# Kernel optimization log

Measured on AMD Instinct MI355X. Metric: run time of the kernel, lower is better.

Reference implementation:

```python
import jax, jax.numpy as jnp
import numpy as np

EPS_LN = 1e-12
EPS_BN = 1e-5


def layernorm(x, w, b):
    u = jnp.mean(x, axis=-1, keepdims=True)
    s = jnp.mean((x - u) ** 2, axis=-1, keepdims=True)
    return w * ((x - u) / jnp.sqrt(s + EPS_LN)) + b


def reps_block(x, ln1_w, ln1_b, lin_w, lin_b, ln2_w, ln2_b):
    # GRAPHLayerNorm -> (dropout, identity in eval) -> Linear -> ReLU -> GRAPHLayerNorm
    h = layernorm(x, ln1_w, ln1_b)
    h = jax.nn.relu(jnp.einsum('bnd,od->bno', h, lin_w) + lin_b)
    return layernorm(h, ln2_w, ln2_b)


def attend(x):
    # full dense self-attention: softmax(x x^T) x ; dropout is identity in eval
    scores = jnp.einsum('bnd,bmd->bnm', x, x)  # [B,4096,4096]
    attn = jax.nn.softmax(scores, axis=-1)
    return jnp.einsum('bnm,bmd->bnd', attn, x)


def setup_inputs() -> dict:
    key = jax.random.key(0)
    ks = jax.random.split(key, 8)
    B, C, H, W = 4, 512, 64, 64
    D = 512
    inp = {
        'T1': jax.random.normal(ks[0], (B, C, H, W), jnp.float32),
        'T2': jax.random.normal(ks[1], (B, C, H, W), jnp.float32),
        'w_conv3': jax.random.normal(ks[2], (1024, 1024, 3, 3), jnp.float32) * 0.01,
        'w_conv1': jax.random.normal(ks[3], (512, 1024, 1, 1), jnp.float32) * 0.03,
        'bn_gamma': jnp.ones((512,), jnp.float32),
        'bn_beta': jnp.zeros((512,), jnp.float32),
        'bn_mean': jnp.zeros((512,), jnp.float32),
        'bn_var': jnp.ones((512,), jnp.float32),
        'ln1_w': jnp.ones((D,), jnp.float32),
        'ln1_b': jnp.zeros((D,), jnp.float32),
        'lin_w': jax.random.normal(ks[4], (D, D), jnp.float32) * 0.04,
        'lin_b': jnp.zeros((D,), jnp.float32),
        'ln2_w': jnp.ones((D,), jnp.float32),
        'ln2_b': jnp.zeros((D,), jnp.float32),
    }
    return inp


def reference(T1, T2, w_conv3, w_conv1, bn_gamma, bn_beta, bn_mean, bn_var,
              ln1_w, ln1_b, lin_w, lin_b, ln2_w, ln2_b):
    B = T1.shape[0]
    X = jnp.concatenate((T1, T2), axis=1)  # [B,1024,64,64]
    dn = ('NCHW', 'OIHW', 'NCHW')
    X = jax.lax.conv_general_dilated(X, w_conv3, (1, 1), ((1, 1), (1, 1)), dimension_numbers=dn)
    X = jax.lax.conv_general_dilated(X, w_conv1, (1, 1), ((0, 0), (0, 0)), dimension_numbers=dn)  # [B,512,64,64]
    # BatchNorm (eval, running stats) + ReLU
    inv = (bn_gamma / jnp.sqrt(bn_var + EPS_BN))[None, :, None, None]
    X = jax.nn.relu(X * inv + (bn_beta - bn_mean * bn_gamma / jnp.sqrt(bn_var + EPS_BN))[None, :, None, None])
    x = X.transpose(0, 2, 3, 1).reshape(B, 4096, 512)
    # block 1
    rel = attend(x)
    rel = reps_block(x + rel, ln1_w, ln1_b, lin_w, lin_b, ln2_w, ln2_b)
    # block 2 (original code reuses self.reps_graph, i.e. SAME params)
    rel1 = attend(rel)
    rel1 = reps_block(rel + rel1, ln1_w, ln1_b, lin_w, lin_b, ln2_w, ln2_b)
    return rel1.reshape(B, 64, 64, 512).transpose(0, 3, 1, 2)  # [B,512,64,64]
```

## Files before the change

### kernel.cpp

```cpp
#include <hip/hip_runtime.h>
#include <stdint.h>

typedef float f32x4 __attribute__((ext_vector_type(4)));
typedef __bf16 bf16x8 __attribute__((ext_vector_type(8)));
typedef unsigned short u16;
typedef unsigned short u16x8 __attribute__((ext_vector_type(8)));
typedef unsigned short u16x4 __attribute__((ext_vector_type(4)));

__device__ __forceinline__ float bf2f(u16 u){ unsigned int i = ((unsigned int)u)<<16; float f; __builtin_memcpy(&f,&i,4); return f; }
__device__ __forceinline__ u16 f2bf(float f){ unsigned int i; __builtin_memcpy(&i,&f,4); i += 0x7FFFu + ((i>>16)&1u); return (u16)(i>>16); }
__device__ __forceinline__ u16 f2h(float f){ _Float16 h = (_Float16)f; u16 b; __builtin_memcpy(&b,&h,2); return b; }
__device__ __forceinline__ float h2f(u16 b){ _Float16 h; __builtin_memcpy(&h,&b,2); return (float)h; }

__device__ __forceinline__ void gld16(const void* g, void* l){
  __builtin_amdgcn_global_load_lds(
      (const __attribute__((address_space(1))) void*)(uintptr_t)g,
      (__attribute__((address_space(3))) void*)(unsigned int)(uintptr_t)l, 16, 0, 0);
}

__global__ __launch_bounds__(256) void pad_interior(const float* __restrict__ T1,
                                                    const float* __restrict__ T2,
                                                    u16* __restrict__ Xpad){
  const int n = blockIdx.z, ct = blockIdx.y, pt = blockIdx.x;
  const int t = threadIdx.x;
  const int c0 = ct*64, p0 = pt*64;
  const float* src = (c0 < 512) ? (T1 + ((long)n*512 + c0)*4096)
                                : (T2 + ((long)n*512 + (c0-512))*4096);
  __shared__ u16 lds[64][66];
  #pragma unroll
  for (int i=0;i<4;i++){
    int c = i*16 + (t>>4);
    int ch = t&15;
    float4 v = *(const float4*)(src + (long)c*4096 + p0 + ch*4);
    int p = ch*4;
    lds[p+0][c] = f2bf(v.x); lds[p+1][c] = f2bf(v.y);
    lds[p+2][c] = f2bf(v.z); lds[p+3][c] = f2bf(v.w);
  }
  __syncthreads();
  #pragma unroll
  for (int i=0;i<8;i++){
    int p = i*8 + (t>>5);
    int c2 = t&31;
    int pix = p0 + p; int yy = (pix>>6)+1, xx = (pix&63)+1;
    ushort2 val; val.x = lds[p][2*c2]; val.y = lds[p][2*c2+1];
    *(ushort2*)(Xpad + (((long)n*66 + yy)*66 + xx)*1024 + c0 + 2*c2) = val;
  }
}

__global__ __launch_bounds__(256) void prep_w3(const float* __restrict__ w3, u16* __restrict__ wk3t){
  const int o = blockIdx.x; const int t = threadIdx.x;
  __shared__ u16 lds[9216];
  const float* src = w3 + (long)o*9216;
  #pragma unroll
  for (int i=0;i<9;i++){
    int j = i*256 + t;
    float4 v = *(const float4*)(src + j*4);
    lds[j*4+0]=f2bf(v.x); lds[j*4+1]=f2bf(v.y); lds[j*4+2]=f2bf(v.z); lds[j*4+3]=f2bf(v.w);
  }
  __syncthreads();
  u16* dst = wk3t + (long)o*9216;
  #pragma unroll
  for (int i=0;i<36;i++){
    int j = i*256 + t; int tp = j>>10, ci = j&1023;
    dst[j] = lds[ci*9+tp];
  }
}

__global__ void prep_w1(const float* __restrict__ w1, const float* __restrict__ bg,
                        const float* __restrict__ bv, u16* __restrict__ w1t){
  long i = (long)blockIdx.x*256 + threadIdx.x;
  int o = (int)(i>>10);
  float inv = bg[o] / sqrtf(bv[o] + 1e-5f);
  w1t[i] = f2bf(w1[i]*inv);
}

__global__ void prep_bias1(const float* __restrict__ bg, const float* __restrict__ bb,
                           const float* __restrict__ bm, const float* __restrict__ bv,
                           float* __restrict__ bias1){
  int o = blockIdx.x*256+threadIdx.x;
  float inv = bg[o]/sqrtf(bv[o]+1e-5f);
  bias1[o] = bb[o] - bm[o]*inv;
}

__global__ void cvt_bf(const float* __restrict__ s, u16* __restrict__ d){
  long i = (long)blockIdx.x*256 + threadIdx.x;
  d[i] = f2bf(s[i]);
}

__global__ __launch_bounds__(256) void row_norm(const u16* __restrict__ x, float* __restrict__ nrm){
  const int row = blockIdx.x*4 + (threadIdx.x>>6);
  const int lane = threadIdx.x & 63;
  u16x8 q = *(const u16x8*)(x + (long)row*512 + lane*8);
  float s = 0.f;
  #pragma unroll
  for (int j=0;j<8;j++){ float f = bf2f(q[j]); s += f*f; }
  #pragma unroll
  for (int off=32; off; off>>=1) s += __shfl_xor(s, off);
  if (lane==0) nrm[row] = s;
}

__global__ __launch_bounds__(256) void transpose_bf(const u16* __restrict__ src, u16* __restrict__ dst,
                                                    int R, int C, long sStr, long dStr){
  const int z = blockIdx.z;
  src += (long)z*sStr; dst += (long)z*dStr;
  const int r0 = blockIdx.x*64, c0 = blockIdx.y*64;
  const int t = threadIdx.x;
  __shared__ u16 lds[64][66];
  #pragma unroll
  for (int i=0;i<4;i++){
    int r = i*16 + (t>>4), ch = t&15;
    ushort4 v = *(const ushort4*)(src + (long)(r0+r)*C + c0 + ch*4);
    lds[r][ch*4+0]=v.x; lds[r][ch*4+1]=v.y; lds[r][ch*4+2]=v.z; lds[r][ch*4+3]=v.w;
  }
  __syncthreads();
  #pragma unroll
  for (int i=0;i<4;i++){
    int c = i*16 + (t>>4), ch = t&15;
    ushort4 v;
    v.x = lds[ch*4+0][c]; v.y = lds[ch*4+1][c]; v.z = lds[ch*4+2][c]; v.w = lds[ch*4+3][c];
    *(ushort4*)(dst + (long)(c0+c)*R + r0 + ch*4) = v;
  }
}

__global__ __launch_bounds__(256) void transpose_bf_f32(const u16* __restrict__ src, float* __restrict__ dst){
  const int z = blockIdx.z;
  src += (long)z*4096*512; dst += (long)z*512*4096;
  const int r0 = blockIdx.x*64, c0 = blockIdx.y*64;
  const int t = threadIdx.x;
  __shared__ u16 lds[64][66];
  #pragma unroll
  for (int i=0;i<4;i++){
    int r = i*16 + (t>>4), ch = t&15;
    ushort4 v = *(const ushort4*)(src + (long)(r0+r)*512 + c0 + ch*4);
    lds[r][ch*4+0]=v.x; lds[r][ch*4+1]=v.y; lds[r][ch*4+2]=v.z; lds[r][ch*4+3]=v.w;
  }
  __syncthreads();
  #pragma unroll
  for (int i=0;i<4;i++){
    int c = i*16 + (t>>4), ch = t&15;
    float4 v;
    v.x = bf2f(lds[ch*4+0][c]); v.y = bf2f(lds[ch*4+1][c]);
    v.z = bf2f(lds[ch*4+2][c]); v.w = bf2f(lds[ch*4+3][c]);
    *(float4*)(dst + (long)(c0+c)*4096 + r0 + ch*4) = v;
  }
}

template<int EPI, int CONV>
__global__ __launch_bounds__(512, 2) void gemm256(
    const u16* __restrict__ A, const u16* __restrict__ Bt, void* __restrict__ Cv,
    int K, int lda, int ldb, int ldc, const float* __restrict__ srow,
    float2* __restrict__ spart)
{
  extern __shared__ u16 sm[];
  const int t = threadIdx.x;
  const int lane = t & 63;
  const int wid = t >> 6;
  const int wr = wid >> 2, wc = wid & 3;

  const int orig = blockIdx.y * gridDim.x + blockIdx.x;
  const int cpx = (gridDim.x * gridDim.y) >> 3;
  const int swz = (orig & 7) * cpx + (orig >> 3);
  const int bx = swz % gridDim.x;
  const int by = swz / gridDim.x;
  const long m0 = (long)by * 256, n0 = (long)bx * 256;

  const int row0 = t >> 2;
  const int cs0  = (t & 3) ^ ((row0 >> 1) & 3);

  const u16 *aB0, *aB1;
  if (CONV) {
    long m_ = m0 + row0;
    long pb0 = ((long)((int)(m_>>12)*66 + (int)((m_>>6)&63)))*66 + (int)(m_&63);
    m_ = m0 + row0 + 128;
    long pb1 = ((long)((int)(m_>>12)*66 + (int)((m_>>6)&63)))*66 + (int)(m_&63);
    aB0 = A + pb0*1024 + cs0*8;
    aB1 = A + pb1*1024 + cs0*8;
  } else {
    aB0 = A + (m0 + row0)*(long)lda + cs0*8;
    aB1 = A + (m0 + row0 + 128)*(long)lda + cs0*8;
  }
  const u16* bB0 = Bt + (n0 + row0)*(long)ldb + cs0*8;
  const u16* bB1 = Bt + (n0 + row0 + 128)*(long)ldb + cs0*8;

  auto issueA = [&](int sub, long aoff){
    u16* d = sm + sub*8192 + t*8;
    gld16(aB0 + aoff, d);
    gld16(aB1 + aoff, d + 4096);
  };
  auto issueB = [&](int sub, long boff){
    u16* d = sm + 32768 + sub*8192 + t*8;
    gld16(bB0 + boff, d);
    gld16(bB1 + boff, d + 4096);
  };
  auto conv_aoff = [&](int tile)->long {
    int kb = tile << 6;
    int tap = kb >> 10;
    int cb  = kb & 1023;
    int ky = (tap >= 6) ? 2 : (tap >= 3 ? 1 : 0);
    int kx = tap - ky*3;
    return (long)(ky*66 + kx)*1024 + cb;
  };

  const int frow = lane & 15;
  const int elemoff = (((lane>>4) ^ ((frow>>1)&3)) << 3);
  const int rAoff = (wr*128 + frow)*32 + elemoff;
  const int rBoff = (wc*64  + frow)*32 + elemoff;

  f32x4 acc[8][4] = {};

  {
    long a0 = CONV ? conv_aoff(0) : 0L;
    issueA(0, a0);
    issueB(0, 0);
    issueA(1, a0 + 32);
    issueB(1, 32);
  }

  const int NT = K >> 6;
  for (int tile = 0; tile < NT; ++tile) {
    const int b = tile & 1;
    const int nb2 = b ^ 1;
    const bool lastT = (tile == NT-1);
    long aoffN = 0, boffN = 0;
    if (!lastT) {
      aoffN = CONV ? conv_aoff(tile+1) : (long)(tile+1)*64;
      boffN = (long)(tile+1)*64;
    }

    asm volatile("s_waitcnt vmcnt(4)" ::: "memory");
    __builtin_amdgcn_s_barrier();
    __builtin_amdgcn_sched_barrier(0);

    {
      const u16* pA = sm + (b*2+0)*8192 + rAoff;
      const u16* pB = sm + 32768 + (b*2+0)*8192 + rBoff;
      bf16x8 bf[4];
      #pragma unroll
      for (int i=0;i<4;i++) bf[i] = *(const bf16x8*)(pB + i*512);
      {
        bf16x8 a[4];
        #pragma unroll
        for (int i=0;i<4;i++) a[i] = *(const bf16x8*)(pA + i*512);
        if (!lastT) issueA(nb2*2+0, aoffN);
        __builtin_amdgcn_s_setprio(1);
        #pragma unroll
        for (int mi=0;mi<4;mi++)
          #pragma unroll
          for (int ni=0;ni<4;ni++)
            acc[mi][ni] = __builtin_amdgcn_mfma_f32_16x16x32_bf16(a[mi], bf[ni], acc[mi][ni],0,0,0);
        __builtin_amdgcn_s_setprio(0);
      }
      {
        bf16x8 a[4];
        #pragma unroll
        for (int i=0;i<4;i++) a[i] = *(const bf16x8*)(pA + (4+i)*512);
        if (!lastT) issueB(nb2*2+0, boffN);
        __builtin_amdgcn_s_setprio(1);
        #pragma unroll
        for (int mi=0;mi<4;mi++)
          #pragma unroll
          for (int ni=0;ni<4;ni++)
            acc[4+mi][ni] = __builtin_amdgcn_mfma_f32_16x16x32_bf16(a[mi], bf[ni], acc[4+mi][ni],0,0,0);
        __builtin_amdgcn_s_setprio(0);
      }
    }

    if (lastT) asm volatile("s_waitcnt vmcnt(0)" ::: "memory");
    else       asm volatile("s_waitcnt vmcnt(4)" ::: "memory");
    __builtin_amdgcn_s_barrier();
    __builtin_amdgcn_sched_barrier(0);

    {
      const u16* pA = sm + (b*2+1)*8192 + rAoff;
      const u16* pB = sm + 32768 + (b*2+1)*8192 + rBoff;
      bf16x8 bf[4];
      #pragma unroll
      for (int i=0;i<4;i++) bf[i] = *(const bf16x8*)(pB + i*512);
      {
        bf16x8 a[4];
        #pragma unroll
        for (int i=0;i<4;i++) a[i] = *(const bf16x8*)(pA + i*512);
        if (!lastT) issueA(nb2*2+1, aoffN + 32);
        __builtin_amdgcn_s_setprio(1);
        #pragma unroll
        for (int mi=0;mi<4;mi++)
          #pragma unroll
          for (int ni=0;ni<4;ni++)
            acc[mi][ni] = __builtin_amdgcn_mfma_f32_16x16x32_bf16(a[mi], bf[ni], acc[mi][ni],0,0,0);
        __builtin_amdgcn_s_setprio(0);
      }
      {
        bf16x8 a[4];
        #pragma unroll
        for (int i=0;i<4;i++) a[i] = *(const bf16x8*)(pA + (4+i)*512);
        if (!lastT) issueB(nb2*2+1, boffN + 32);
        __builtin_amdgcn_s_setprio(1);
        #pragma unroll
        for (int mi=0;mi<4;mi++)
          #pragma unroll
          for (int ni=0;ni<4;ni++)
            acc[4+mi][ni] = __builtin_amdgcn_mfma_f32_16x16x32_bf16(a[mi], bf[ni], acc[4+mi][ni],0,0,0);
        __builtin_amdgcn_s_setprio(0);
      }
    }
  }

  const int crow0 = wr*128 + ((lane>>4)<<2);
  const int ccol0 = wc*64 + frow;
  if (EPI == 3) {
    #pragma unroll
    for (int mi=0;mi<8;mi++){
      #pragma unroll
      for (int r=0;r<4;r++){
        long row = m0 + crow0 + mi*16 + r;
        float sr = srow[row];
        float sv0 = acc[mi][0][r]-sr, sv1 = acc[mi][1][r]-sr;
        float sv2 = acc[mi][2][r]-sr, sv3 = acc[mi][3][r]-sr;
        u16* cb = (u16*)Cv + row*(long)ldc + n0 + ccol0;
        cb[0] = f2h(sv0); cb[16] = f2h(sv1); cb[32] = f2h(sv2); cb[48] = f2h(sv3);
        float M4 = fmaxf(fmaxf(sv0,sv1), fmaxf(sv2,sv3));
        M4 = fmaxf(M4, __shfl_xor(M4,1)); M4 = fmaxf(M4, __shfl_xor(M4,2));
        M4 = fmaxf(M4, __shfl_xor(M4,4)); M4 = fmaxf(M4, __shfl_xor(M4,8));
        float e = __expf(sv0-M4)+__expf(sv1-M4)+__expf(sv2-M4)+__expf(sv3-M4);
        e += __shfl_xor(e,1); e += __shfl_xor(e,2);
        e += __shfl_xor(e,4); e += __shfl_xor(e,8);
        if ((lane&15)==0) spart[row*64 + (n0>>6) + wc] = make_float2(M4, e);
      }
    }
  } else {
    #pragma unroll
    for (int mi=0;mi<8;mi++){
      #pragma unroll
      for (int ni=0;ni<4;ni++){
        long col = n0 + ccol0 + ni*16;
        #pragma unroll
        for (int r=0;r<4;r++){
          long row = m0 + crow0 + mi*16 + r;
          ((u16*)Cv)[row*(long)ldc + col] = f2bf(acc[mi][ni][r]);
        }
      }
    }
  }
}

__global__ __launch_bounds__(256) void finalize_lse(const float2* __restrict__ sp,
                                                    float2* __restrict__ out){
  const int row = blockIdx.x*4 + (threadIdx.x>>6);
  const int lane = threadIdx.x & 63;
  float2 p = sp[row*64 + lane];
  float M = p.x;
  #pragma unroll
  for (int off=32; off; off>>=1) M = fmaxf(M, __shfl_xor(M, off));
  float e = p.y * __expf(p.x - M);
  #pragma unroll
  for (int off=32; off; off>>=1) e += __shfl_xor(e, off);
  if (lane==0) out[row] = make_float2(M, 1.0f/e);
}

template<int EPI>
__global__ __launch_bounds__(256, 2) void gemm_bt(
    const u16* __restrict__ A, const u16* __restrict__ Bt,
    void* __restrict__ Cv, const float* __restrict__ bias,
    int K, int lda, int ldb, int ldc)
{
  const int t = threadIdx.x;
  const int lane = t & 63;
  const int w = t >> 6;
  const int wr = w >> 1, wc = w & 1;
  const long m0 = (long)blockIdx.y * 128;
  const long n0 = (long)blockIdx.x * 128;

  __shared__ u16 lA[128*32];
  __shared__ u16 lB[128*32];

  const u16* aS0 = A + (m0 + (t>>2))*(long)lda + (t&3)*8;
  const u16* aS1 = aS0 + 64*(long)lda;
  const u16* bS0 = Bt + (n0 + (t>>2))*(long)ldb + (t&3)*8;
  const u16* bS1 = bS0 + 64*(long)ldb;
  u16* dA0 = lA + t*8; u16* dA1 = lA + 2048 + t*8;
  u16* dB0 = lB + t*8; u16* dB1 = lB + 2048 + t*8;

  f32x4 acc[4][4] = {};
  const int frow = lane & 15, kq = (lane >> 4) * 8;
  const u16* rA = lA + (wr*64 + frow)*32 + kq;
  const u16* rB = lB + (wc*64 + frow)*32 + kq;

  for (int kb = 0; kb < K; kb += 32) {
    gld16(aS0 + kb, dA0); gld16(aS1 + kb, dA1);
    gld16(bS0 + kb, dB0); gld16(bS1 + kb, dB1);
    __syncthreads();
    bf16x8 af[4], bfr[4];
    #pragma unroll
    for (int i=0;i<4;i++) af[i]  = *(const bf16x8*)(rA + i*512);
    #pragma unroll
    for (int i=0;i<4;i++) bfr[i] = *(const bf16x8*)(rB + i*512);
    #pragma unroll
    for (int mi=0;mi<4;mi++)
      #pragma unroll
      for (int ni=0;ni<4;ni++)
        acc[mi][ni] = __builtin_amdgcn_mfma_f32_16x16x32_bf16(af[mi], bfr[ni], acc[mi][ni], 0,0,0);
    __syncthreads();
  }

  const int crow0 = wr*64 + ((lane>>4)<<2);
  const int ccol0 = wc*64 + (lane&15);
  #pragma unroll
  for (int mi=0;mi<4;mi++){
    #pragma unroll
    for (int ni=0;ni<4;ni++){
      long col = n0 + ccol0 + ni*16;
      float bv = (EPI==1) ? bias[col] : 0.0f;
      #pragma unroll
      for (int r=0;r<4;r++){
        long row = m0 + crow0 + mi*16 + r;
        float v = acc[mi][ni][r];
        if (EPI==1){ v += bv; v = v > 0.0f ? v : 0.0f; }
        ((u16*)Cv)[row*(long)ldc + col] = f2bf(v);
      }
    }
  }
}

__global__ __launch_bounds__(512, 2) void pv2(
    const u16* __restrict__ S0a, const u16* __restrict__ S1a,
    const u16* __restrict__ S2a, const u16* __restrict__ S3a,
    const float2* __restrict__ rstats, const u16* __restrict__ xT,
    u16* __restrict__ attb)
{
  extern __shared__ u16 pm[];
  u16* lA = pm;
  u16* lB = pm + 2048;
  const int z = blockIdx.y;
  const u16* Sz = (z==0)?S0a:(z==1)?S1a:(z==2)?S2a:S3a;
  const long ZS = 4096L*512;
  const u16* Bt = xT + (long)z*ZS;
  u16* C = attb + (long)z*ZS;
  const int swz = (blockIdx.x & 7)*16 + (blockIdx.x >> 3);
  const long m0 = (long)swz * 32;
  const int t = threadIdx.x;
  const int lane = t & 63, w = t >> 6;

  const int brow = t >> 3;
  const int bch  = t & 7;
  const u16* bS = Bt + (long)brow*4096 + ((bch ^ (brow & 7)) * 8);
  u16* bD = lB + t*8;

  const int arow = t >> 4;
  const int aq   = t & 15;
  float2 st = rstats[(long)z*4096 + m0 + arow];
  const float Mrow = st.x, iLrow = st.y;
  const u16* aS = Sz + (m0 + arow)*4096L + aq*4;
  u16* aD = lA + arow*64 + (((aq>>1) ^ (arow & 7)) * 8) + (aq & 1)*4;

  const int fr = lane & 15;
  const int eor = lane & 7;
  const int co0 = (((lane>>4)     ^ eor) * 8);
  const int co1 = (((4+(lane>>4)) ^ eor) * 8);
  const u16* rA = lA + fr*64;
  const u16* rB = lB + (w*64 + fr)*64;

  f32x4 acc[2][4] = {};

  for (int kb = 0; kb < 4096; kb += 64) {
    #pragma unroll
    for (int p = 0; p < 8; p++)
      gld16(bS + (long)p*262144 + kb, bD + p*4096);
    {
      u16x4 q = *(const u16x4*)(aS + kb);
      u16x4 o;
      #pragma unroll
      for (int j=0;j<4;j++)
        o[j] = f2bf(__expf(h2f(q[j]) - Mrow) * iLrow);
      *(u16x4*)aD = o;
    }
    __syncthreads();
    #pragma unroll
    for (int kk = 0; kk < 2; kk++) {
      const int co = kk ? co1 : co0;
      bf16x8 af0 = *(const bf16x8*)(rA + co);
      bf16x8 af1 = *(const bf16x8*)(rA + 1024 + co);
      #pragma unroll
      for (int ni=0;ni<4;ni++){
        bf16x8 bv = *(const bf16x8*)(rB + ni*1024 + co);
        acc[0][ni] = __builtin_amdgcn_mfma_f32_16x16x32_bf16(af0, bv, acc[0][ni],0,0,0);
        acc[1][ni] = __builtin_amdgcn_mfma_f32_16x16x32_bf16(af1, bv, acc[1][ni],0,0,0);
      }
    }
    __syncthreads();
  }

  #pragma unroll
  for (int mi=0;mi<2;mi++){
    #pragma unroll
    for (int ni=0;ni<4;ni++){
      long col = w*64 + ni*16 + fr;
      #pragma unroll
      for (int r=0;r<4;r++){
        long row = m0 + mi*16 + (lane>>4)*4 + r;
        C[row*512 + col] = f2bf(acc[mi][ni][r]);
      }
    }
  }
}

template<int ADD>
__global__ __launch_bounds__(256) void ln_row(
    const u16* __restrict__ X, const u16* __restrict__ Y,
    const float* __restrict__ w, const float* __restrict__ b,
    u16* __restrict__ outB)
{
  const long row = blockIdx.x;
  const int t = threadIdx.x, lane = t&63, wv = t>>6;
  ushort2 xv = *(const ushort2*)(X + row*512 + t*2);
  float v0 = bf2f(xv.x), v1 = bf2f(xv.y);
  if (ADD){
    ushort2 yv = *(const ushort2*)(Y + row*512 + t*2);
    v0 += bf2f(yv.x); v1 += bf2f(yv.y);
  }
  float s = v0+v1, q = v0*v0 + v1*v1;
  #pragma unroll
  for (int off=32; off; off>>=1){ s += __shfl_xor(s,off); q += __shfl_xor(q,off); }
  __shared__ float red[8];
  if (lane==0){ red[wv]=s; red[4+wv]=q; }
  __syncthreads();
  s = red[0]+red[1]+red[2]+red[3];
  q = red[4]+red[5]+red[6]+red[7];
  const float u = s*(1.0f/512.0f);
  const float var = q*(1.0f/512.0f) - u*u;
  const float inv = rsqrtf(var + 1e-12f);
  const int c = t*2;
  float o0 = (v0-u)*inv*w[c]   + b[c];
  float o1 = (v1-u)*inv*w[c+1] + b[c+1];
  ushort2 ov; ov.x=f2bf(o0); ov.y=f2bf(o1);
  *(ushort2*)(outB + row*512 + c) = ov;
}

extern "C" void kernel_launch(void* const* d_in, const int* in_sizes, int n_in,
                              void* d_out, int out_size, void* d_ws, size_t ws_size,
                              hipStream_t stream) {
  const float* T1   = (const float*)d_in[0];
  const float* T2   = (const float*)d_in[1];
  const float* w3   = (const float*)d_in[2];
  const float* w1   = (const float*)d_in[3];
  const float* bg   = (const float*)d_in[4];
  const float* bb   = (const float*)d_in[5];
  const float* bm   = (const float*)d_in[6];
  const float* bv   = (const float*)d_in[7];
  const float* ln1w = (const float*)d_in[8];
  const float* ln1b = (const float*)d_in[9];
  const float* linw = (const float*)d_in[10];
  const float* linb = (const float*)d_in[11];
  const float* ln2w = (const float*)d_in[12];
  const float* ln2b = (const float*)d_in[13];

  hipFuncSetAttribute(reinterpret_cast<const void*>(gemm256<0,1>),
                      hipFuncAttributeMaxDynamicSharedMemorySize, 131072);
  hipFuncSetAttribute(reinterpret_cast<const void*>(gemm256<3,0>),
                      hipFuncAttributeMaxDynamicSharedMemorySize, 131072);
  hipFuncSetAttribute(reinterpret_cast<const void*>(pv2),
                      hipFuncAttributeMaxDynamicSharedMemorySize, 69632);

  char* ws = (char*)d_ws;
  size_t off = 0;
  auto alloc = [&](size_t bytes)->char* {
    char* p = ws + off;
    off += (bytes + 255) & ~(size_t)255;
    return p;
  };
  const size_t XPAD_B = 4L*66*66*1024*2;
  u16*   Xpad  = (u16*)  alloc(XPAD_B);
  u16*   wk3t  = (u16*)  alloc(1024L*9216*2);
  u16*   w1t   = (u16*)  alloc(512L*1024*2);
  u16*   lint  = (u16*)  alloc(512L*512*2);
  float* bias1 = (float*)alloc(512*4);
  float* nrm   = (float*)alloc(16384L*4);
  float2* Spart= (float2*)alloc(4096L*64*8);
  float2* rst  = (float2*)alloc(4L*4096*8);
  u16*   Y1    = (u16*)  alloc(16384L*1024*2);
  u16*   x0    = (u16*)  alloc(16384L*512*2);
  u16*   xT    = (u16*)  alloc(4L*512*4096*2);
  u16*   Sreg  = (u16*)  alloc(2L*4096*4096*2);
  u16*   attb  = (u16*)  alloc(16384L*512*2);
  u16*   h     = (u16*)  alloc(16384L*512*2);
  u16*   g     = (u16*)  alloc(16384L*512*2);
  u16*   rel1  = (u16*)  alloc(16384L*512*2);
  u16*   S0    = Y1;
  u16*   S1    = Sreg;
  u16*   S2    = Sreg + 4096L*4096;
  u16*   S3    = Xpad;
  if (off > ws_size) return;

  const long ZS = 4096L*512;

  hipMemsetAsync(Xpad, 0, XPAD_B, stream);
  pad_interior<<<dim3(64,16,4), 256, 0, stream>>>(T1, T2, Xpad);
  prep_w3<<<1024, 256, 0, stream>>>(w3, wk3t);
  prep_w1<<<2048, 256, 0, stream>>>(w1, bg, bv, w1t);
  prep_bias1<<<2, 256, 0, stream>>>(bg, bb, bm, bv, bias1);
  cvt_bf<<<1024, 256, 0, stream>>>(linw, lint);

  gemm256<0,1><<<dim3(4,64), 512, 131072, stream>>>(Xpad, wk3t, (void*)Y1, 9216, 0, 9216, 1024,
                                                    nullptr, nullptr);
  gemm_bt<1><<<dim3(4,128), 256, 0, stream>>>(Y1, w1t, (void*)x0, bias1, 1024, 1024, 1024, 512);

  u16* Sz[4] = {S0, S1, S2, S3};
  auto attend = [&](const u16* xin){
    transpose_bf<<<dim3(64,8,4), 256, 0, stream>>>(xin, xT, 4096, 512, ZS, ZS);
    row_norm<<<4096, 256, 0, stream>>>(xin, nrm);
    for (int z=0; z<4; z++){
      const u16* xz = xin + (long)z*ZS;
      gemm256<3,0><<<dim3(16,16), 512, 131072, stream>>>(xz, xz, (void*)Sz[z], 512, 512, 512, 4096,
                                                         nrm + (long)z*4096, Spart);
      finalize_lse<<<1024, 256, 0, stream>>>(Spart, rst + (long)z*4096);
    }
    pv2<<<dim3(128,4), 512, 69632, stream>>>(S0, S1, S2, S3, rst, xT, attb);
  };

  attend(x0);
  ln_row<1><<<16384, 256, 0, stream>>>(x0, attb, ln1w, ln1b, h);
  gemm_bt<1><<<dim3(4,128), 256, 0, stream>>>(h, lint, (void*)g, linb, 512, 512, 512, 512);
  ln_row<0><<<16384, 256, 0, stream>>>(g, nullptr, ln2w, ln2b, rel1);

  attend(rel1);
  ln_row<1><<<16384, 256, 0, stream>>>(rel1, attb, ln1w, ln1b, h);
  gemm_bt<1><<<dim3(4,128), 256, 0, stream>>>(h, lint, (void*)g, linb, 512, 512, 512, 512);
  ln_row<0><<<16384, 256, 0, stream>>>(g, nullptr, ln2w, ln2b, x0);

  transpose_bf_f32<<<dim3(64,8,4), 256, 0, stream>>>(x0, (float*)d_out);
}
```

Baseline: 974.7 us.

## Retile attention PV kernel to 128x128 tiles with XCD-aware block mapping

Replaces the 32-row x 512-col PV kernel with a 128x128 output tile kernel (256 threads, 4x4 MFMA per wave, K step 32). The grid is 1D with the batch index derived from the XCD slot, so each batch's tiles stay on a pair of XCDs for L2 locality. It also register-prefetches the next fp16 score chunk before the barrier. The aim is more MFMA work per LDS load and better L2 reuse of xT. The cost is that each 128-row block of probabilities is now exponentiated four times, once per column tile, where before it was done once.

```diff
diff --git a/kernel.cpp b/kernel.cpp
--- a/kernel.cpp
+++ b/kernel.cpp
@@ -421,82 +421,95 @@
   }
 }
 
-__global__ __launch_bounds__(512, 2) void pv2(
+__global__ __launch_bounds__(256, 2) void pv3(
     const u16* __restrict__ S0a, const u16* __restrict__ S1a,
     const u16* __restrict__ S2a, const u16* __restrict__ S3a,
     const float2* __restrict__ rstats, const u16* __restrict__ xT,
     u16* __restrict__ attb)
 {
-  extern __shared__ u16 pm[];
-  u16* lA = pm;
-  u16* lB = pm + 2048;
-  const int z = blockIdx.y;
+  const int L = blockIdx.x;
+  const int xcd = L & 7;
+  const int z = xcd >> 1;
+  const int tile = ((L >> 3) << 1) + (xcd & 1);
+  const int bx = tile & 3, by = tile >> 2;
   const u16* Sz = (z==0)?S0a:(z==1)?S1a:(z==2)?S2a:S3a;
   const long ZS = 4096L*512;
   const u16* Bt = xT + (long)z*ZS;
   u16* C = attb + (long)z*ZS;
-  const int swz = (blockIdx.x & 7)*16 + (blockIdx.x >> 3);
-  const long m0 = (long)swz * 32;
+  const long m0 = (long)by*128, n0 = (long)bx*128;
+
   const int t = threadIdx.x;
   const int lane = t & 63, w = t >> 6;
-
-  const int brow = t >> 3;
-  const int bch  = t & 7;
-  const u16* bS = Bt + (long)brow*4096 + ((bch ^ (brow & 7)) * 8);
-  u16* bD = lB + t*8;
-
-  const int arow = t >> 4;
-  const int aq   = t & 15;
-  float2 st = rstats[(long)z*4096 + m0 + arow];
-  const float Mrow = st.x, iLrow = st.y;
-  const u16* aS = Sz + (m0 + arow)*4096L + aq*4;
-  u16* aD = lA + arow*64 + (((aq>>1) ^ (arow & 7)) * 8) + (aq & 1)*4;
-
-  const int fr = lane & 15;
-  const int eor = lane & 7;
-  const int co0 = (((lane>>4)     ^ eor) * 8);
-  const int co1 = (((4+(lane>>4)) ^ eor) * 8);
-  const u16* rA = lA + fr*64;
-  const u16* rB = lB + (w*64 + fr)*64;
-
-  f32x4 acc[2][4] = {};
-
-  for (int kb = 0; kb < 4096; kb += 64) {
-    #pragma unroll
-    for (int p = 0; p < 8; p++)
-      gld16(bS + (long)p*262144 + kb, bD + p*4096);
-    {
-      u16x4 q = *(const u16x4*)(aS + kb);
-      u16x4 o;
-      #pragma unroll
-      for (int j=0;j<4;j++)
-        o[j] = f2bf(__expf(h2f(q[j]) - Mrow) * iLrow);
-      *(u16x4*)aD = o;
+  const int wr = w >> 1, wc = w & 1;
+
+  __shared__ u16 lA[128*32];
+  __shared__ u16 lB[128*32];
+
+  const int row0 = t >> 2;
+  const int cs0  = (t & 3) ^ ((row0 >> 1) & 3);
+
+  const u16* bS0 = Bt + (n0 + row0)*4096L + cs0*8;
+  const u16* bS1 = bS0 + 64*4096L;
+  u16* dB0 = lB + t*8; u16* dB1 = lB + 2048 + t*8;
+
+  const u16* aS0 = Sz + (m0 + row0)*4096L + (t&3)*8;
+  const u16* aS1 = aS0 + 64*4096L;
+  u16* aD0 = lA + row0*32 + cs0*8;
+  u16* aD1 = lA + 2048 + row0*32 + cs0*8;
+
+  float2 st0 = rstats[(long)z*4096 + m0 + row0];
+  float2 st1 = rstats[(long)z*4096 + m0 + row0 + 64];
+  const float M0 = st0.x, iL0 = st0.y;
+  const float M1 = st1.x, iL1 = st1.y;
+
+  const int frow = lane & 15;
+  const int elemoff = (((lane>>4) ^ ((frow>>1)&3)) << 3);
+  const u16* rA = lA + (wr*64 + frow)*32 + elemoff;
+  const u16* rB = lB + (wc*64 + frow)*32 + elemoff;
+
+  f32x4 acc[4][4] = {};
+
+  u16x8 a0 = *(const u16x8*)(aS0);
+  u16x8 a1 = *(const u16x8*)(aS1);
+
+  for (int kb = 0; kb < 4096; kb += 32) {
+    gld16(bS0 + kb, dB0); gld16(bS1 + kb, dB1);
+    bf16x8 pa0, pa1;
+    #pragma unroll
+    for (int j=0;j<8;j++){
+      pa0[j] = (__bf16)(__expf(h2f(a0[j]) - M0) * iL0);
+      pa1[j] = (__bf16)(__expf(h2f(a1[j]) - M1) * iL1);
+    }
+    *(bf16x8*)aD0 = pa0;
+    *(bf16x8*)aD1 = pa1;
+    if (kb + 32 < 4096){
+      a0 = *(const u16x8*)(aS0 + kb + 32);
+      a1 = *(const u16x8*)(aS1 + kb + 32);
     }
     __syncthreads();
-    #pragma unroll
-    for (int kk = 0; kk < 2; kk++) {
-      const int co = kk ? co1 : co0;
-      bf16x8 af0 = *(const bf16x8*)(rA + co);
-      bf16x8 af1 = *(const bf16x8*)(rA + 1024 + co);
-      #pragma unroll
-      for (int ni=0;ni<4;ni++){
-        bf16x8 bv = *(const bf16x8*)(rB + ni*1024 + co);
-        acc[0][ni] = __builtin_amdgcn_mfma_f32_16x16x32_bf16(af0, bv, acc[0][ni],0,0,0);
-        acc[1][ni] = __builtin_amdgcn_mfma_f32_16x16x32_bf16(af1, bv, acc[1][ni],0,0,0);
-      }
-    }
+    bf16x8 af[4], bfr[4];
+    #pragma unroll
+    for (int i=0;i<4;i++) af[i]  = *(const bf16x8*)(rA + i*512);
+    #pragma unroll
+    for (int i=0;i<4;i++) bfr[i] = *(const bf16x8*)(rB + i*512);
+    #pragma unroll
+    for (int mi=0;mi<4;mi++)
+      #pragma unroll
+      for (int ni=0;ni<4;ni++)
+        acc[mi][ni] = __builtin_amdgcn_mfma_f32_16x16x32_bf16(af[mi], bfr[ni], acc[mi][ni], 0,0,0);
     __syncthreads();
   }
 
-  #pragma unroll
-  for (int mi=0;mi<2;mi++){
+  const int crow0 = wr*64 + ((lane>>4)<<2);
+  const int ccol0 = wc*64 + frow;
+  #pragma unroll
+  for (int mi=0;mi<4;mi++){
     #pragma unroll
     for (int ni=0;ni<4;ni++){
-      long col = w*64 + ni*16 + fr;
+      long col = n0 + ccol0 + ni*16;
       #pragma unroll
       for (int r=0;r<4;r++){
-        long row = m0 + mi*16 + (lane>>4)*4 + r;
+        long row = m0 + crow0 + mi*16 + r;
         C[row*512 + col] = f2bf(acc[mi][ni][r]);
       }
     }
@@ -557,8 +570,6 @@
                       hipFuncAttributeMaxDynamicSharedMemorySize, 131072);
   hipFuncSetAttribute(reinterpret_cast<const void*>(gemm256<3,0>),
                       hipFuncAttributeMaxDynamicSharedMemorySize, 131072);
-  hipFuncSetAttribute(reinterpret_cast<const void*>(pv2),
-                      hipFuncAttributeMaxDynamicSharedMemorySize, 69632);
 
   char* ws = (char*)d_ws;
   size_t off = 0;
@@ -613,7 +624,7 @@
                                                          nrm + (long)z*4096, Spart);
       finalize_lse<<<1024, 256, 0, stream>>>(Spart, rst + (long)z*4096);
     }
-    pv2<<<dim3(128,4), 512, 69632, stream>>>(S0, S1, S2, S3, rst, xT, attb);
+    pv3<<<512, 256, 0, stream>>>(S0, S1, S2, S3, rst, xT, attb);
   };
 
   attend(x0);
```

New measurement: 1.012 ms. 1.04x slower.

## Rewrite PV kernel with 64-row tiles, double-buffered LDS, and XCD-aware mapping

Applied to the files above, without the earlier changes.

Replaces the P·V attention kernel with a version that processes 64 query rows per block instead of 32, doubling reuse of each loaded V tile. It double-buffers both the V tile and the softmax-probability tile in LDS, prefetching the next K step while the MFMAs run, so the loop needs one barrier per iteration instead of two. Blocks are also remapped so each XCD handles a single batch slice. The cost is 144KB of LDS and more accumulator registers per block, which limits the kernel to one block per CU and halves the grid to 256 blocks.

```diff
diff --git a/kernel.cpp b/kernel.cpp
--- a/kernel.cpp
+++ b/kernel.cpp
@@ -5,7 +5,6 @@
 typedef __bf16 bf16x8 __attribute__((ext_vector_type(8)));
 typedef unsigned short u16;
 typedef unsigned short u16x8 __attribute__((ext_vector_type(8)));
-typedef unsigned short u16x4 __attribute__((ext_vector_type(4)));
 
 __device__ __forceinline__ float bf2f(u16 u){ unsigned int i = ((unsigned int)u)<<16; float f; __builtin_memcpy(&f,&i,4); return f; }
 __device__ __forceinline__ u16 f2bf(float f){ unsigned int i; __builtin_memcpy(&i,&f,4); i += 0x7FFFu + ((i>>16)&1u); return (u16)(i>>16); }
@@ -421,82 +420,103 @@
   }
 }
 
-__global__ __launch_bounds__(512, 2) void pv2(
+__global__ __launch_bounds__(512) void pv4(
     const u16* __restrict__ S0a, const u16* __restrict__ S1a,
     const u16* __restrict__ S2a, const u16* __restrict__ S3a,
     const float2* __restrict__ rstats, const u16* __restrict__ xT,
     u16* __restrict__ attb)
 {
   extern __shared__ u16 pm[];
-  u16* lA = pm;
-  u16* lB = pm + 2048;
-  const int z = blockIdx.y;
+  const int L = blockIdx.x;
+  const int xcd = L & 7;
+  const int z = xcd >> 1;
+  const int qt = ((L >> 3) << 1) + (xcd & 1);
+  const long m0 = (long)qt * 64;
   const u16* Sz = (z==0)?S0a:(z==1)?S1a:(z==2)?S2a:S3a;
   const long ZS = 4096L*512;
   const u16* Bt = xT + (long)z*ZS;
   u16* C = attb + (long)z*ZS;
-  const int swz = (blockIdx.x & 7)*16 + (blockIdx.x >> 3);
-  const long m0 = (long)swz * 32;
+
   const int t = threadIdx.x;
   const int lane = t & 63, w = t >> 6;
 
   const int brow = t >> 3;
   const int bch  = t & 7;
   const u16* bS = Bt + (long)brow*4096 + ((bch ^ (brow & 7)) * 8);
-  u16* bD = lB + t*8;
-
-  const int arow = t >> 4;
-  const int aq   = t & 15;
-  float2 st = rstats[(long)z*4096 + m0 + arow];
-  const float Mrow = st.x, iLrow = st.y;
-  const u16* aS = Sz + (m0 + arow)*4096L + aq*4;
-  u16* aD = lA + arow*64 + (((aq>>1) ^ (arow & 7)) * 8) + (aq & 1)*4;
+  const u16* aS = Sz + (m0 + brow)*4096L + bch*8;
+  float2 st = rstats[(long)z*4096 + m0 + brow];
+  const float Mr = st.x, iLr = st.y;
+  const int aDoff = brow*64 + ((bch ^ (brow & 7)) * 8);
+
+  auto issueB = [&](int buf, long koff){
+    u16* d = pm + buf*32768 + t*8;
+    #pragma unroll
+    for (int p=0;p<8;p++)
+      gld16(bS + (long)p*64*4096 + koff, d + p*4096);
+  };
 
   const int fr = lane & 15;
-  const int eor = lane & 7;
-  const int co0 = (((lane>>4)     ^ eor) * 8);
-  const int co1 = (((4+(lane>>4)) ^ eor) * 8);
-  const u16* rA = lA + fr*64;
-  const u16* rB = lB + (w*64 + fr)*64;
-
-  f32x4 acc[2][4] = {};
-
-  for (int kb = 0; kb < 4096; kb += 64) {
-    #pragma unroll
-    for (int p = 0; p < 8; p++)
-      gld16(bS + (long)p*262144 + kb, bD + p*4096);
-    {
-      u16x4 q = *(const u16x4*)(aS + kb);
-      u16x4 o;
-      #pragma unroll
-      for (int j=0;j<4;j++)
-        o[j] = f2bf(__expf(h2f(q[j]) - Mrow) * iLrow);
-      *(u16x4*)aD = o;
+  const int kg = lane >> 4;
+
+  f32x4 acc[4][4] = {};
+
+  u16x8 sreg = *(const u16x8*)(aS);
+  issueB(0, 0);
+  {
+    bf16x8 pa;
+    #pragma unroll
+    for (int j=0;j<8;j++) pa[j] = (__bf16)(__expf(h2f(sreg[j]) - Mr) * iLr);
+    *(bf16x8*)(pm + 65536 + aDoff) = pa;
+  }
+  __syncthreads();
+
+  for (int kt = 0; kt < 64; ++kt){
+    const int c = kt & 1, nb = c ^ 1;
+    const bool last = (kt == 63);
+    if (!last){
+      sreg = *(const u16x8*)(aS + (kt+1)*64);
+      issueB(nb, (long)(kt+1)*64);
+    }
+    const u16* A_ = pm + 65536 + c*4096;
+    const u16* B_ = pm + c*32768 + w*4096;
+    #pragma unroll
+    for (int s=0;s<2;s++){
+      bf16x8 af[4], bfr[4];
+      #pragma unroll
+      for (int mi=0;mi<4;mi++){
+        int row = mi*16 + fr;
+        int ch = (s*4 + kg) ^ (row & 7);
+        af[mi] = *(const bf16x8*)(A_ + row*64 + ch*8);
+      }
+      #pragma unroll
+      for (int ni=0;ni<4;ni++){
+        int row = ni*16 + fr;
+        int ch = (s*4 + kg) ^ (row & 7);
+        bfr[ni] = *(const bf16x8*)(B_ + row*64 + ch*8);
+      }
+      #pragma unroll
+      for (int mi=0;mi<4;mi++)
+        #pragma unroll
+        for (int ni=0;ni<4;ni++)
+          acc[mi][ni] = __builtin_amdgcn_mfma_f32_16x16x32_bf16(af[mi], bfr[ni], acc[mi][ni],0,0,0);
+    }
+    if (!last){
+      bf16x8 pa;
+      #pragma unroll
+      for (int j=0;j<8;j++) pa[j] = (__bf16)(__expf(h2f(sreg[j]) - Mr) * iLr);
+      *(bf16x8*)(pm + 65536 + nb*4096 + aDoff) = pa;
     }
     __syncthreads();
-    #pragma unroll
-    for (int kk = 0; kk < 2; kk++) {
-      const int co = kk ? co1 : co0;
-      bf16x8 af0 = *(const bf16x8*)(rA + co);
-      bf16x8 af1 = *(const bf16x8*)(rA + 1024 + co);
-      #pragma unroll
-      for (int ni=0;ni<4;ni++){
-        bf16x8 bv = *(const bf16x8*)(rB + ni*1024 + co);
-        acc[0][ni] = __builtin_amdgcn_mfma_f32_16x16x32_bf16(af0, bv, acc[0][ni],0,0,0);
-        acc[1][ni] = __builtin_amdgcn_mfma_f32_16x16x32_bf16(af1, bv, acc[1][ni],0,0,0);
-      }
-    }
-    __syncthreads();
-  }
-
-  #pragma unroll
-  for (int mi=0;mi<2;mi++){
+  }
+
+  #pragma unroll
+  for (int mi=0;mi<4;mi++){
     #pragma unroll
     for (int ni=0;ni<4;ni++){
       long col = w*64 + ni*16 + fr;
       #pragma unroll
       for (int r=0;r<4;r++){
-        long row = m0 + mi*16 + (lane>>4)*4 + r;
+        long row = m0 + mi*16 + kg*4 + r;
         C[row*512 + col] = f2bf(acc[mi][ni][r]);
       }
     }
@@ -557,8 +577,8 @@
                       hipFuncAttributeMaxDynamicSharedMemorySize, 131072);
   hipFuncSetAttribute(reinterpret_cast<const void*>(gemm256<3,0>),
                       hipFuncAttributeMaxDynamicSharedMemorySize, 131072);
-  hipFuncSetAttribute(reinterpret_cast<const void*>(pv2),
-                      hipFuncAttributeMaxDynamicSharedMemorySize, 69632);
+  hipFuncSetAttribute(reinterpret_cast<const void*>(pv4),
+                      hipFuncAttributeMaxDynamicSharedMemorySize, 147456);
 
   char* ws = (char*)d_ws;
   size_t off = 0;
@@ -613,7 +633,7 @@
                                                          nrm + (long)z*4096, Spart);
       finalize_lse<<<1024, 256, 0, stream>>>(Spart, rst + (long)z*4096);
     }
-    pv2<<<dim3(128,4), 512, 69632, stream>>>(S0, S1, S2, S3, rst, xT, attb);
+    pv4<<<256, 512, 147456, stream>>>(S0, S1, S2, S3, rst, xT, attb);
   };
 
   attend(x0);
```

After: 938.0 us. -3.8%, faster.
